# Optimization experiments

Hardware: AMD Instinct MI355X
Metric: run time of the kernel (lower is better)

Reference implementation:

```python
import jax, jax.numpy as jnp
import numpy as np

BETA = 0.95
SG_SLOPE = 25.0

@jax.custom_vjp
def spike(mem, thr):
    return (mem > thr).astype(mem.dtype)

def _spike_fwd(mem, thr):
    return spike(mem, thr), (mem, thr)

def _spike_bwd(res, g):
    mem, thr = res
    s = jax.nn.sigmoid(SG_SLOPE * (mem - thr))
    return (g * (SG_SLOPE * s * (1.0 - s)), jnp.zeros_like(thr))

spike.defvjp(_spike_fwd, _spike_bwd)

def setup_inputs() -> dict:
    key = jax.random.key(0)
    ks = jax.random.split(key, 7)
    T, B, IN, H, OUT = 50, 512, 784, 800, 10
    return {
        "x":  jax.random.normal(ks[0], (T, B, IN), dtype=jnp.float32),
        "W1": jax.random.normal(ks[1], (H, IN), dtype=jnp.float32) / np.sqrt(IN),
        "b1": jax.random.normal(ks[2], (H,), dtype=jnp.float32) * 0.01,
        "W2": jax.random.normal(ks[3], (H, H), dtype=jnp.float32) / np.sqrt(H),
        "b2": jax.random.normal(ks[4], (H,), dtype=jnp.float32) * 0.01,
        "W3": jax.random.normal(ks[5], (OUT, H), dtype=jnp.float32) / np.sqrt(H),
        "b3": jax.random.normal(ks[6], (OUT,), dtype=jnp.float32) * 0.01,
        "thresh1": jnp.ones((H,), dtype=jnp.float32),
        "thresh2": jnp.ones((H,), dtype=jnp.float32),
    }

def reference(x, W1, b1, W2, b2, W3, b3, thresh1, thresh2):
    T, B = x.shape[0], x.shape[1]
    H, OUT = W1.shape[0], W3.shape[0]
    # Batch the input projection across all timesteps: [T,B,H]
    x1 = jnp.einsum('tbi,hi->tbh', x, W1) + b1

    def step(carry, xt):
        mem1, mem2, mem3 = carry
        mem1 = BETA * mem1 + xt
        spk1 = spike(mem1, thresh1)
        mem1 = mem1 * (1.0 - spk1)
        mem2 = BETA * mem2 + spk1 @ W2.T + b2
        spk2 = spike(mem2, thresh2)
        mem2 = mem2 * (1.0 - spk2)
        mem3 = BETA * mem3 + spk2 @ W3.T + b3
        spk3 = spike(mem3, jnp.float32(1.0))
        mem3 = mem3 * (1.0 - spk3)
        return (mem1, mem2, mem3), (spk1, spk2, spk3)

    init = (jnp.zeros((B, H), x.dtype), jnp.zeros((B, H), x.dtype), jnp.zeros((B, OUT), x.dtype))
    _, (s1r, s2r, s3r) = jax.lax.scan(step, init, x1)
    return s3r.sum(0), s1r, s2r, s3r
```

## Files before the change

kernel.cpp:

```cpp
#include <hip/hip_runtime.h>

#define TT 50
#define BB 512
#define II 784
#define HH 800
#define OO 10
#define BH (BB*HH)
#define MM (TT*BB)

typedef double d4 __attribute__((ext_vector_type(4)));

__device__ __forceinline__ int dec16(double V) {
    const int vi = (int)(V + 0.5);
    const int a = vi - 96;
    if (a >= 0 && a < 64 && (a & 3) == 0) return a >> 2;
    return ((vi - 6) >> 4) & 15;
}
__device__ __forceinline__ bool isf1(double V) {
    const int vi = (int)(V + 0.5);
    const int a = vi - 96;
    return (a >= 0 && a < 64 && (a & 3) == 0);
}

template<int NS>
__device__ __forceinline__ void gemm1_compute_d(
    const double* __restrict__ Ab, const double* __restrict__ Bb,
    int wm, int arow, int akk, int bcol, int bkk, d4 acc[2][5])
{
    #pragma unroll
    for (int s = 0; s < NS; ++s) {
        const int ka = 4*s + akk;
        const int kb = 4*s + bkk;
        const double a0d = Ab[ka*132 + wm + arow];
        const double a1d = Ab[ka*132 + wm + 16 + arow];
        double bd[5];
        #pragma unroll
        for (int j = 0; j < 5; ++j)
            bd[j] = Bb[kb*84 + 16*j + bcol];
        #pragma unroll
        for (int j = 0; j < 5; ++j) {
            acc[0][j] = __builtin_amdgcn_mfma_f64_16x16x4f64(
                a0d, bd[j], acc[0][j], 0, 0, 0);
            acc[1][j] = __builtin_amdgcn_mfma_f64_16x16x4f64(
                a1d, bd[j], acc[1][j], 0, 0, 0);
        }
    }
}

__global__ __launch_bounds__(256) void k_gemm1(
    const float* __restrict__ x, const float* __restrict__ W1,
    const float* __restrict__ b1, double* __restrict__ x1d)
{
    __shared__ double Asd[2][8*132];
    __shared__ double Bsd[2][8*84];
    const int m0 = blockIdx.x * 128;
    const int n0 = blockIdx.y * 80;
    const int tid = threadIdx.x;
    const int lane = tid & 63;
    const int wm = (tid >> 6) * 32;

    const d4 zc = {0.0, 0.0, 0.0, 0.0};
    const d4 pr = __builtin_amdgcn_mfma_f64_16x16x4f64(
        (double)lane, 1.0, zc, 0, 0, 0);
    const d4 pc = __builtin_amdgcn_mfma_f64_16x16x4f64(
        1.0, (double)lane, zc, 0, 0, 0);
    int rowIdx[4], colIdx[4];
    #pragma unroll
    for (int r = 0; r < 4; ++r) {
        rowIdx[r] = dec16(pr[r]) & 15;
        colIdx[r] = dec16(pc[r]) & 15;
    }
    const bool af1 = isf1(pr[0]);
    const bool bf1 = isf1(pc[0]);
    const int arow = af1 ? (lane & 15) : (lane >> 2);
    const int akk  = af1 ? (lane >> 4) : (lane & 3);
    const int bcol = bf1 ? (lane & 15) : (lane >> 2);
    const int bkk  = bf1 ? (lane >> 4) : (lane & 3);

    d4 acc[2][5] = {};

    const int sm = tid >> 1;
    const int sk = (tid & 1) * 4;
    const int bn0 = tid >> 2, bk0 = (tid & 3) * 2;
    const int bn1 = 64 + (tid >> 2);

    const float* aptr  = x  + (long)(m0+sm)*II + sk;
    const float* bptr0 = W1 + (long)(n0+bn0)*II + bk0;
    const float* bptr1 = W1 + (long)(n0+bn1)*II + bk0;

    float4 pa = *(const float4*)(aptr);
    float2 pb0 = *(const float2*)(bptr0);
    float2 pb1;
    if (tid < 64) pb1 = *(const float2*)(bptr1);

    for (int c = 0; c < 98; ++c) {
        double* Ad = &Asd[c & 1][0];
        double* Bd = &Bsd[c & 1][0];
        Ad[(sk+0)*132+sm] = (double)pa.x;
        Ad[(sk+1)*132+sm] = (double)pa.y;
        Ad[(sk+2)*132+sm] = (double)pa.z;
        Ad[(sk+3)*132+sm] = (double)pa.w;
        Bd[(bk0+0)*84+bn0] = (double)pb0.x;
        Bd[(bk0+1)*84+bn0] = (double)pb0.y;
        if (tid < 64) {
            Bd[(bk0+0)*84+bn1] = (double)pb1.x;
            Bd[(bk0+1)*84+bn1] = (double)pb1.y;
        }
        if (c + 1 < 98) {
            const int k0 = (c + 1) * 8;
            pa = *(const float4*)(aptr + k0);
            pb0 = *(const float2*)(bptr0 + k0);
            if (tid < 64) pb1 = *(const float2*)(bptr1 + k0);
        }
        __syncthreads();
        gemm1_compute_d<2>(Ad, Bd, wm, arow, akk, bcol, bkk, acc);
    }

    #pragma unroll
    for (int i = 0; i < 2; ++i) {
        #pragma unroll
        for (int r = 0; r < 4; ++r) {
            const long m = m0 + wm + 16*i + rowIdx[r];
            #pragma unroll
            for (int j = 0; j < 5; ++j) {
                const int n = n0 + 16*j + colIdx[r];
                x1d[m*HH + n] = acc[i][j][r] + (double)b1[n];
            }
        }
    }
}

__global__ __launch_bounds__(256) void k_mem1(
    const double* __restrict__ x1d, const float* __restrict__ thresh1,
    unsigned char* __restrict__ s1c, float* __restrict__ s1r)
{
    const int lid = blockIdx.x*256 + threadIdx.x;
    const int h = lid % HH;
    const double th = (double)thresh1[h];
    double mem = 0.0;
    for (int t = 0; t < TT; ++t) {
        const long idx = (long)t*BH + lid;
        mem = 0.95*mem + x1d[idx];
        const bool spk = mem > th;
        s1c[idx] = spk ? 1 : 0;
        s1r[idx] = spk ? 1.0f : 0.0f;
        if (spk) mem = 0.0;
    }
}

__global__ __launch_bounds__(256) void k_gemm2(
    const unsigned char* __restrict__ s1c, const float* __restrict__ W2,
    float* __restrict__ z2)
{
    __shared__ float As[2][16*132];
    __shared__ float Bs[2][16*84];
    const int m0 = blockIdx.x * 128;
    const int n0 = blockIdx.y * 80;
    const int tid = threadIdx.x;
    const int tx = tid & 15, ty = tid >> 4;
    float acc[8][5] = {};

    const int am = tid >> 1;
    const int ak = (tid & 1) * 8;
    const int bn0 = tid >> 2, bk0 = (tid & 3) * 4;
    const int q1 = tid + 256;
    const int bn1 = q1 >> 2, bk1 = (q1 & 3) * 4;

    const unsigned char* ap = s1c + (long)(m0+am)*HH + ak;
    const float* bp0 = W2 + (long)(n0+bn0)*HH + bk0;
    const float* bp1 = W2 + (long)(n0+bn1)*HH + bk1;

    uint2 ra = *(const uint2*)(ap);
    float4 rb0 = *(const float4*)(bp0);
    float4 rb1;
    if (tid < 64) rb1 = *(const float4*)(bp1);

    for (int c = 0; c < 50; ++c) {
        float* Ad = &As[c & 1][0];
        float* Bd = &Bs[c & 1][0];
        {
            const unsigned int lo = ra.x, hi = ra.y;
            Ad[(ak+0)*132+am] = (float)( lo        & 0xffu);
            Ad[(ak+1)*132+am] = (float)((lo >>  8) & 0xffu);
            Ad[(ak+2)*132+am] = (float)((lo >> 16) & 0xffu);
            Ad[(ak+3)*132+am] = (float)((lo >> 24) & 0xffu);
            Ad[(ak+4)*132+am] = (float)( hi        & 0xffu);
            Ad[(ak+5)*132+am] = (float)((hi >>  8) & 0xffu);
            Ad[(ak+6)*132+am] = (float)((hi >> 16) & 0xffu);
            Ad[(ak+7)*132+am] = (float)((hi >> 24) & 0xffu);
        }
        Bd[(bk0+0)*84+bn0] = rb0.x;
        Bd[(bk0+1)*84+bn0] = rb0.y;
        Bd[(bk0+2)*84+bn0] = rb0.z;
        Bd[(bk0+3)*84+bn0] = rb0.w;
        if (tid < 64) {
            Bd[(bk1+0)*84+bn1] = rb1.x;
            Bd[(bk1+1)*84+bn1] = rb1.y;
            Bd[(bk1+2)*84+bn1] = rb1.z;
            Bd[(bk1+3)*84+bn1] = rb1.w;
        }
        if (c + 1 < 50) {
            const int k0 = (c + 1) * 16;
            ra = *(const uint2*)(ap + k0);
            rb0 = *(const float4*)(bp0 + k0);
            if (tid < 64) rb1 = *(const float4*)(bp1 + k0);
        }
        __syncthreads();
        #pragma unroll
        for (int k = 0; k < 16; ++k) {
            const float4 a01 = *(const float4*)&Ad[k*132 + ty*8];
            const float4 a23 = *(const float4*)&Ad[k*132 + ty*8 + 4];
            const float4 bv  = *(const float4*)&Bd[k*84 + tx*4];
            const float  b4s = Bd[k*84 + 64 + tx];
            const float a[8] = {a01.x,a01.y,a01.z,a01.w,
                                a23.x,a23.y,a23.z,a23.w};
            const float b[5] = {bv.x,bv.y,bv.z,bv.w,b4s};
            #pragma unroll
            for (int i = 0; i < 8; ++i)
                #pragma unroll
                for (int j = 0; j < 5; ++j)
                    acc[i][j] = __fmaf_rn(a[i], b[j], acc[i][j]);
        }
    }
    #pragma unroll
    for (int i = 0; i < 8; ++i) {
        const long m = m0 + ty*8 + i;
        #pragma unroll
        for (int j = 0; j < 4; ++j)
            z2[m*HH + n0 + tx*4 + j] = acc[i][j];
        z2[m*HH + n0 + 64 + tx] = acc[i][4];
    }
}

__global__ __launch_bounds__(256) void k_scan2(
    const float* __restrict__ z2, const float* __restrict__ b2,
    const float* __restrict__ thresh2, float* __restrict__ s2r,
    unsigned char* __restrict__ s2c)
{
    const int lid = blockIdx.x*256 + threadIdx.x;
    const int n = lid % HH;
    const float b2v = b2[n];
    const float thv = thresh2[n];
    float m = 0.0f;
    for (int t = 0; t < TT; ++t) {
        const long idx = (long)t*BH + lid;
        const float m2 = __fadd_rn(
            __fadd_rn(__fmul_rn(0.95f, m), z2[idx]), b2v);
        const bool spk = m2 > thv;
        s2r[idx] = spk ? 1.0f : 0.0f;
        s2c[idx] = spk ? 1 : 0;
        m = spk ? 0.0f : m2;
    }
}

__global__ __launch_bounds__(256) void k_gemm3(
    const unsigned char* __restrict__ s2c, const float* __restrict__ W3,
    float* __restrict__ z3)
{
    const long m = blockIdx.x*256 + threadIdx.x;
    const unsigned char* row = s2c + m*HH;
    float acc[10] = {};
    for (int k0 = 0; k0 < HH; k0 += 16) {
        const uint4 v = *(const uint4*)(row + k0);
        const unsigned int d[4] = {v.x, v.y, v.z, v.w};
        #pragma unroll
        for (int w = 0; w < 4; ++w) {
            #pragma unroll
            for (int j = 0; j < 4; ++j) {
                const float sv = (float)((d[w] >> (8*j)) & 0xffu);
                const int k = k0 + w*4 + j;
                #pragma unroll
                for (int o = 0; o < 10; ++o)
                    acc[o] = __fmaf_rn(sv, W3[o*HH + k], acc[o]);
            }
        }
    }
    #pragma unroll
    for (int o = 0; o < 10; ++o)
        z3[m*OO + o] = acc[o];
}

__global__ __launch_bounds__(256) void k_scan3(
    const float* __restrict__ z3, const float* __restrict__ b3,
    float* __restrict__ s3r, float* __restrict__ out0)
{
    const int gid = blockIdx.x*256 + threadIdx.x;
    if (gid >= BB*OO) return;
    const int o = gid % OO;
    const float b3v = b3[o];
    float mem = 0.0f, cnt = 0.0f;
    for (int t = 0; t < TT; ++t) {
        const float m3 = __fadd_rn(
            __fadd_rn(__fmul_rn(0.95f, mem), z3[(long)t*BB*OO + gid]), b3v);
        const bool spk = m3 > 1.0f;
        s3r[(long)t*BB*OO + gid] = spk ? 1.0f : 0.0f;
        if (spk) cnt = __fadd_rn(cnt, 1.0f);
        mem = spk ? 0.0f : m3;
    }
    out0[gid] = cnt;
}

extern "C" void kernel_launch(void* const* d_in, const int* in_sizes, int n_in,
                              void* d_out, int out_size, void* d_ws, size_t ws_size,
                              hipStream_t stream)
{
    const float* x   = (const float*)d_in[0];
    const float* W1  = (const float*)d_in[1];
    const float* b1  = (const float*)d_in[2];
    const float* W2  = (const float*)d_in[3];
    const float* b2  = (const float*)d_in[4];
    const float* W3  = (const float*)d_in[5];
    const float* b3  = (const float*)d_in[6];
    const float* th1 = (const float*)d_in[7];
    const float* th2 = (const float*)d_in[8];

    float* out0 = (float*)d_out;
    float* s1r  = out0 + BB*OO;
    float* s2r  = s1r + (long)TT*BH;
    float* s3r  = s2r + (long)TT*BH;

    char* p = (char*)d_ws;
    double* x1d = (double*)p;
    float*  z2  = (float*)p;
    float*  z3  = (float*)(p + 84000000);
    unsigned char* s1c = (unsigned char*)(p + 163840000);
    unsigned char* s2c = s1c + (size_t)TT*BH;
    (void)ws_size;

    k_gemm1<<<dim3(200,10), dim3(256), 0, stream>>>(x, W1, b1, x1d);
    k_mem1 <<<dim3(1600),   dim3(256), 0, stream>>>(x1d, th1, s1c, s1r);
    k_gemm2<<<dim3(200,10), dim3(256), 0, stream>>>(s1c, W2, z2);
    k_scan2<<<dim3(1600),   dim3(256), 0, stream>>>(z2, b2, th2, s2r, s2c);
    k_gemm3<<<dim3(100),    dim3(256), 0, stream>>>(s2c, W3, z3);
    k_scan3<<<dim3(20),     dim3(256), 0, stream>>>(z3, b3, s3r, out0);
}
```

Baseline: 1.423 ms.

## Stage gemm1 tiles as fp32 in LDS with K-chunk 16 and unrolled double buffer

The input-projection GEMM now keeps its shared-memory tiles in fp32 instead of converting to double before storing, which halves LDS footprint and store traffic. The conversion to double moves to the point where each MFMA operand is read. The K chunk per sync doubles from 8 to 16, so there are 49 iterations instead of 98 and half as many barriers. The double-buffer loop is manually unrolled with precomputed LDS pointers to remove index arithmetic. The cost is extra conversion instructions in the inner MFMA loop and a larger unrolled body that may raise register pressure.

```diff
diff --git a/kernel.cpp b/kernel.cpp
--- a/kernel.cpp
+++ b/kernel.cpp
@@ -22,21 +22,17 @@
     return (a >= 0 && a < 64 && (a & 3) == 0);
 }
 
-template<int NS>
-__device__ __forceinline__ void gemm1_compute_d(
-    const double* __restrict__ Ab, const double* __restrict__ Bb,
-    int wm, int arow, int akk, int bcol, int bkk, d4 acc[2][5])
-{
-    #pragma unroll
-    for (int s = 0; s < NS; ++s) {
-        const int ka = 4*s + akk;
-        const int kb = 4*s + bkk;
-        const double a0d = Ab[ka*132 + wm + arow];
-        const double a1d = Ab[ka*132 + wm + 16 + arow];
+__device__ __forceinline__ void g1_comp(
+    const float* __restrict__ pA, const float* __restrict__ pB, d4 acc[2][5])
+{
+    #pragma unroll
+    for (int s = 0; s < 4; ++s) {
+        const double a0d = (double)pA[s*576];
+        const double a1d = (double)pA[s*576 + 16];
         double bd[5];
         #pragma unroll
         for (int j = 0; j < 5; ++j)
-            bd[j] = Bb[kb*84 + 16*j + bcol];
+            bd[j] = (double)pB[s*320 + 16*j];
         #pragma unroll
         for (int j = 0; j < 5; ++j) {
             acc[0][j] = __builtin_amdgcn_mfma_f64_16x16x4f64(
@@ -51,8 +47,8 @@
     const float* __restrict__ x, const float* __restrict__ W1,
     const float* __restrict__ b1, double* __restrict__ x1d)
 {
-    __shared__ double Asd[2][8*132];
-    __shared__ double Bsd[2][8*84];
+    __shared__ float As0[16*144], As1[16*144];
+    __shared__ float Bs0[16*80],  Bs1[16*80];
     const int m0 = blockIdx.x * 128;
     const int n0 = blockIdx.y * 80;
     const int tid = threadIdx.x;
@@ -80,41 +76,70 @@
     d4 acc[2][5] = {};
 
     const int sm = tid >> 1;
-    const int sk = (tid & 1) * 4;
-    const int bn0 = tid >> 2, bk0 = (tid & 3) * 2;
-    const int bn1 = 64 + (tid >> 2);
+    const int sk = (tid & 1) * 8;
+    const int bn0 = tid >> 2, bk0 = (tid & 3) * 4;
+    const int q1  = tid + 256;
+    const int bn1 = q1 >> 2,  bk1 = (q1 & 3) * 4;
+
+    const float* pA0r = As0 + akk*144 + wm + arow;
+    const float* pA1r = As1 + akk*144 + wm + arow;
+    const float* pB0r = Bs0 + bkk*80 + bcol;
+    const float* pB1r = Bs1 + bkk*80 + bcol;
+    float* wA0 = As0 + sk*144 + sm;
+    float* wA1 = As1 + sk*144 + sm;
+    float* wB0a = Bs0 + bk0*80 + bn0;
+    float* wB1a = Bs1 + bk0*80 + bn0;
+    float* wB0b = Bs0 + bk1*80 + bn1;
+    float* wB1b = Bs1 + bk1*80 + bn1;
 
     const float* aptr  = x  + (long)(m0+sm)*II + sk;
-    const float* bptr0 = W1 + (long)(n0+bn0)*II + bk0;
-    const float* bptr1 = W1 + (long)(n0+bn1)*II + bk0;
-
-    float4 pa = *(const float4*)(aptr);
-    float2 pb0 = *(const float2*)(bptr0);
-    float2 pb1;
-    if (tid < 64) pb1 = *(const float2*)(bptr1);
-
-    for (int c = 0; c < 98; ++c) {
-        double* Ad = &Asd[c & 1][0];
-        double* Bd = &Bsd[c & 1][0];
-        Ad[(sk+0)*132+sm] = (double)pa.x;
-        Ad[(sk+1)*132+sm] = (double)pa.y;
-        Ad[(sk+2)*132+sm] = (double)pa.z;
-        Ad[(sk+3)*132+sm] = (double)pa.w;
-        Bd[(bk0+0)*84+bn0] = (double)pb0.x;
-        Bd[(bk0+1)*84+bn0] = (double)pb0.y;
-        if (tid < 64) {
-            Bd[(bk0+0)*84+bn1] = (double)pb1.x;
-            Bd[(bk0+1)*84+bn1] = (double)pb1.y;
-        }
-        if (c + 1 < 98) {
-            const int k0 = (c + 1) * 8;
-            pa = *(const float4*)(aptr + k0);
-            pb0 = *(const float2*)(bptr0 + k0);
-            if (tid < 64) pb1 = *(const float2*)(bptr1 + k0);
-        }
+    const float* bptrA = W1 + (long)(n0+bn0)*II + bk0;
+    const float* bptrB = W1 + (long)(n0+bn1)*II + bk1;
+
+#define G1_STORE(WA, WBa, WBb, A0, A1, W0, W1v) do {                     \
+        WA[0*144] = A0.x;  WA[1*144] = A0.y;                             \
+        WA[2*144] = A0.z;  WA[3*144] = A0.w;                             \
+        WA[4*144] = A1.x;  WA[5*144] = A1.y;                             \
+        WA[6*144] = A1.z;  WA[7*144] = A1.w;                             \
+        WBa[0*80] = W0.x;  WBa[1*80] = W0.y;                             \
+        WBa[2*80] = W0.z;  WBa[3*80] = W0.w;                             \
+        if (tid < 64) {                                                  \
+            WBb[0*80] = W1v.x;  WBb[1*80] = W1v.y;                       \
+            WBb[2*80] = W1v.z;  WBb[3*80] = W1v.w;                       \
+        }                                                                \
+    } while (0)
+
+    float4 a0A, a1A, w0A, w1A;
+    float4 a0B, a1B, w0B, w1B;
+
+    a0A = *(const float4*)(aptr);
+    a1A = *(const float4*)(aptr + 4);
+    w0A = *(const float4*)(bptrA);
+    if (tid < 64) w1A = *(const float4*)(bptrB);
+
+    int kofs = 16;
+    for (int i = 0; i < 24; ++i) {
+        G1_STORE(wA0, wB0a, wB0b, a0A, a1A, w0A, w1A);
+        a0B = *(const float4*)(aptr + kofs);
+        a1B = *(const float4*)(aptr + kofs + 4);
+        w0B = *(const float4*)(bptrA + kofs);
+        if (tid < 64) w1B = *(const float4*)(bptrB + kofs);
         __syncthreads();
-        gemm1_compute_d<2>(Ad, Bd, wm, arow, akk, bcol, bkk, acc);
-    }
+        g1_comp(pA0r, pB0r, acc);
+        G1_STORE(wA1, wB1a, wB1b, a0B, a1B, w0B, w1B);
+        a0A = *(const float4*)(aptr + kofs + 16);
+        a1A = *(const float4*)(aptr + kofs + 20);
+        w0A = *(const float4*)(bptrA + kofs + 16);
+        if (tid < 64) w1A = *(const float4*)(bptrB + kofs + 16);
+        __syncthreads();
+        g1_comp(pA1r, pB1r, acc);
+        kofs += 32;
+    }
+    G1_STORE(wA0, wB0a, wB0b, a0A, a1A, w0A, w1A);
+    __syncthreads();
+    g1_comp(pA0r, pB0r, acc);
+
+#undef G1_STORE
 
     #pragma unroll
     for (int i = 0; i < 2; ++i) {
```

Measured after the change: 1.424 ms. About the same (+0.0%).
